# Kernel optimization log

Measured on AMD Instinct MI355X. Metric: run time of the kernel, lower is better.

## Reference

```python
import jax, jax.numpy as jnp
import numpy as np

N_ROOMS = 126          # len(building.rooms)
N = 2 + N_ROOMS        # state dim (reset_iv: 2 + n_rooms)
M = 1 + N_ROOMS        # input dim u = [Tout, Q_watts...]
T = 200000             # number of eval times
DT = 30.0              # seconds between eval points
TOUT_DT = 3600.0       # outside-temp table grid spacing (s)
K = 1700               # table length (covers 1000 + T*DT seconds)
LOAD_MAX = 500.0       # physical_loads_scaling: W/m^2 upper bound


def setup_inputs() -> dict:
    key = jax.random.key(0)
    ks = jax.random.split(key, 6)
    # Stable RC-style state matrix: negative diagonal dominates
    A = 1e-5 * jax.random.normal(ks[0], (N, N), dtype=jnp.float32) - 2e-4 * jnp.eye(N, dtype=jnp.float32)
    B = 1e-6 * jax.random.normal(ks[1], (N, M), dtype=jnp.float32)
    loads = jax.random.normal(ks[2], (2, N_ROOMS), dtype=jnp.float32)   # raw params (pre-sigmoid)
    areas = 10.0 + 40.0 * jax.random.uniform(ks[3], (N_ROOMS,), dtype=jnp.float32)  # room areas m^2
    Tout_vals = 10.0 + 5.0 * jax.random.normal(ks[4], (K,), dtype=jnp.float32)      # hourly Tout table
    t_eval = 1000.0 + DT * jnp.arange(T, dtype=jnp.float32)
    iv = 26.0 * jnp.ones((N, 1), dtype=jnp.float32)
    return {"A": A, "B": B, "loads": loads, "areas": areas,
            "Tout_vals": Tout_vals, "t_eval": t_eval, "iv": iv, "action": 1}


def _interp_tout(vals, t):
    # linear interpolation on a uniform grid starting at t=0 (replaces scipy interp1d)
    pos = t / TOUT_DT
    idx = jnp.clip(jnp.floor(pos).astype(jnp.int32), 0, K - 2)
    w = pos - idx.astype(pos.dtype)
    return vals[idx] * (1.0 - w) + vals[idx + 1] * w


def reference(A, B, loads, areas, Tout_vals, t_eval, iv, action):
    t0 = t_eval[0]
    ts = t_eval - t0
    # _build_loads: sigmoid transform + physical scaling
    lp = jax.nn.sigmoid(loads) * LOAD_MAX
    cool_load, gain_load = lp[0], lp[1]
    # f_ode constants: Q_area = -cool*action + gain; Q_watts = proportional_heating
    Q_watts = (-cool_load * action + gain_load) * areas        # [n_rooms]
    b_q = B[:, 1:] @ Q_watts                                   # [N] constant forcing
    b_T = B[:, 0]                                              # [N] Tout coupling
    x0 = iv[:, 0]

    def f(t, x):
        Tout = _interp_tout(Tout_vals, t + t0)
        return A @ x + b_T * Tout + b_q

    # torchdiffeq method='rk4' -> rk4_alt_step_func (3/8 rule)
    def step(x, tt):
        t, tn = tt
        dt = tn - t
        k1 = f(t, x)
        k2 = f(t + dt / 3.0, x + dt * k1 / 3.0)
        k3 = f(t + dt * 2.0 / 3.0, x + dt * (k2 - k1 / 3.0))
        k4 = f(t + dt, x + dt * (k1 - k2 + k3))
        xn = x + dt * (k1 + 3.0 * (k2 + k3) + k4) / 8.0
        return xn, xn

    _, traj = jax.lax.scan(step, x0, (ts[:-1], ts[1:]))
    out = jnp.concatenate([x0[None, :], traj], axis=0)         # [T, N]
    return out[..., None]                                      # [T, N, 1] matching iv shape
```

## Files before the change

### kernel.cpp

```cpp
#include <hip/hip_runtime.h>

#define N 128
#define NR 126
#define MBCOL 127
#define TSTEPS 200000
#define L1 49
#define C1 4096
#define L2 64
#define C2 64
#define KT 1700

#define OFF_Z     0
#define OFF_S     16384
#define OFF_P     32768
#define OFF_PW2   65536
#define OFF_PW4   81920
#define OFF_PW8   98304
#define OFF_PW16  114688
#define OFF_PW32  131072
#define OFF_Q     147456
#define OFF_WC    180224
#define OFF_ACC   212992
#define OFF_DELTA 737280
#define OFF_BQ    745472
#define OFF_BST   753664
#define OFF_PEH   65536
#define OFF_PEL   75776

typedef float v4f __attribute__((ext_vector_type(4)));
typedef __attribute__((ext_vector_type(8))) short bf16x8;
typedef __attribute__((ext_vector_type(4))) float f32x4;

#define GLD4(dst, p) \
  asm volatile("global_load_dwordx4 %0, %1, off" : "=v"(dst) : "v"(p))
#define PINQ(q) \
  asm volatile("s_waitcnt vmcnt(0)" \
    : "+v"(q[0]),"+v"(q[1]),"+v"(q[2]),"+v"(q[3]), \
      "+v"(q[4]),"+v"(q[5]),"+v"(q[6]),"+v"(q[7]), \
      "+v"(q[8]),"+v"(q[9]),"+v"(q[10]),"+v"(q[11]), \
      "+v"(q[12]),"+v"(q[13]),"+v"(q[14]),"+v"(q[15]))

__device__ __forceinline__ void loadQ16(v4f* qv, const float* pb)
{
  #pragma unroll
  for (int s = 0; s < 16; ++s) GLD4(qv[s], pb + 4*s);
  PINQ(qv);
}

__device__ __forceinline__ void bsplit(float f, unsigned short& h, unsigned short& l)
{
  unsigned int u = __float_as_uint(f);
  unsigned int r = (u + 0x7FFFu + ((u >> 16) & 1u)) >> 16;
  float hf = __uint_as_float(r << 16);
  h = (unsigned short)r;
  float lo = f - hf;
  unsigned int u2 = __float_as_uint(lo);
  unsigned int r2 = (u2 + 0x7FFFu + ((u2 >> 16) & 1u)) >> 16;
  l = (unsigned short)r2;
}

__global__ __launch_bounds__(128) void kPrep(
    const float* __restrict__ A, const float* __restrict__ B,
    const float* __restrict__ loads, const float* __restrict__ areas,
    const float* __restrict__ iv, const int* __restrict__ action,
    float* __restrict__ ws, float* __restrict__ out)
{
  __shared__ float qw[NR];
  __shared__ float ys[4][N];
  __shared__ float qs[4][N];
  int t = threadIdx.x;
  float actf = (float)action[0];
  if (t < NR) {
    float lc = (1.0f / (1.0f + expf(-loads[t]))) * 500.0f;
    float lg = (1.0f / (1.0f + expf(-loads[NR + t]))) * 500.0f;
    qw[t] = (-lc * actf + lg) * areas[t];
  }
  __syncthreads();
  {
    float bq = 0.0f;
    for (int i = 0; i < NR; ++i) bq += B[t * MBCOL + 1 + i] * qw[i];
    ys[0][t] = B[t * MBCOL];
    qs[0][t] = bq;
  }
  __syncthreads();
  for (int s = 1; s < 4; ++s) {
    float ay = 0.0f, aq = 0.0f;
    for (int k = 0; k < N; ++k) {
      float a = A[t * N + k];
      ay += a * ys[s-1][k];
      aq += a * qs[s-1][k];
    }
    ys[s][t] = 30.0f * ay;
    qs[s][t] = 30.0f * aq;
    __syncthreads();
  }
  float vs[5];
  vs[0] = 3.75f * (ys[0][t] + ys[1][t] + ys[2][t]*(1.0f/3.0f) + ys[3][t]*(1.0f/3.0f));
  vs[1] = 3.75f * (3.0f*ys[0][t] + 2.0f*ys[1][t] + ys[2][t]);
  vs[2] = 3.75f * (3.0f*ys[0][t] + ys[1][t]);
  vs[3] = 3.75f * ys[0][t];
  vs[4] = 3.75f * (8.0f*qs[0][t] + 4.0f*qs[1][t] + (4.0f/3.0f)*qs[2][t] + (1.0f/3.0f)*qs[3][t]);
  for (int m = 0; m < 5; ++m) ws[OFF_WC + (m*L1) * N + t] = vs[m];
  for (int i = t; i < N*N; i += 128) ws[OFF_Z + i] = 30.0f * A[i];
  out[t] = iv[t];
}

__device__ __forceinline__ void mmRow(const float* __restrict__ Aw,
                                      const float* __restrict__ Bw,
                                      float* __restrict__ Cw,
                                      float* __restrict__ Cw2,
                                      float* __restrict__ sm)
{
  int t = threadIdx.x, c = t & 127, kh = t >> 7;
  int r = blockIdx.x;
  const float* Ar = Aw + r*N + kh*64;
  const float* Bc = Bw + (kh*64)*N + c;
  float p0=0.f, p1=0.f, p2=0.f, p3=0.f;
  #pragma unroll 4
  for (int s = 0; s < 64; s += 4) {
    const float4 av = *(const float4*)(Ar + s);
    p0 = fmaf(av.x, Bc[(s+0)*N], p0);
    p1 = fmaf(av.y, Bc[(s+1)*N], p1);
    p2 = fmaf(av.z, Bc[(s+2)*N], p2);
    p3 = fmaf(av.w, Bc[(s+3)*N], p3);
  }
  sm[kh*128 + c] = (p0+p1)+(p2+p3);
  __syncthreads();
  if (kh == 0) {
    float v = sm[c] + sm[128 + c];
    Cw[r*N + c] = v;
    if (Cw2) Cw2[r*N + c] = v;
  }
}

__device__ __forceinline__ void polyRow(float* __restrict__ ws,
                                        float* __restrict__ sm)
{
  int t = threadIdx.x, c = t & 127, kh = t >> 7;
  int r = blockIdx.x;
  const float* Z = ws + OFF_Z;
  const float* S = ws + OFF_S;
  const float* Sr = S + r*N + kh*64;
  float x3=0.f, x4=0.f;
  #pragma unroll 4
  for (int s = 0; s < 64; s += 4) {
    const float4 av = *(const float4*)(Sr + s);
    int k = kh*64 + s;
    x3 = fmaf(av.x, Z[(k+0)*N+c], x3); x3 = fmaf(av.y, Z[(k+1)*N+c], x3);
    x3 = fmaf(av.z, Z[(k+2)*N+c], x3); x3 = fmaf(av.w, Z[(k+3)*N+c], x3);
    x4 = fmaf(av.x, S[(k+0)*N+c], x4); x4 = fmaf(av.y, S[(k+1)*N+c], x4);
    x4 = fmaf(av.z, S[(k+2)*N+c], x4); x4 = fmaf(av.w, S[(k+3)*N+c], x4);
  }
  sm[kh*128 + c] = x3;
  sm[256 + kh*128 + c] = x4;
  __syncthreads();
  if (kh == 0) {
    float a3 = sm[c] + sm[128+c];
    float a4 = sm[256+c] + sm[384+c];
    float pv = (r==c ? 1.0f : 0.0f) + Z[r*N+c] + 0.5f*S[r*N+c]
             + (1.0f/6.0f)*a3 + (1.0f/24.0f)*a4;
    ws[OFF_P + r*N + c] = pv;
  }
}

__device__ __forceinline__ void wUnit(const float* __restrict__ Pw,
                                      float* __restrict__ ws,
                                      int uw, int wbase, int wcount,
                                      float* __restrict__ wbuf )
{
  int t = threadIdx.x;
  int np = 5 * wcount;
  for (int i = t; i < 8*N; i += 256) {
    int pl = i >> 7, k = i & 127;
    int p = uw*8 + pl;
    float v = 0.0f;
    if (p < np) {
      int m = p / wcount, kk = p % wcount;
      v = ws[OFF_WC + (m*L1 + kk)*N + k];
    }
    wbuf[pl*N + k] = v;
  }
  __syncthreads();
  int r = t & 127, pg = t >> 7;
  float acc[4] = {0,0,0,0};
  #pragma unroll 2
  for (int k = 0; k < N; k += 4) {
    const float4 av = *(const float4*)(Pw + r*N + k);
    #pragma unroll
    for (int pi = 0; pi < 4; ++pi) {
      const float4 wv = *(const float4*)(wbuf + (pg*4+pi)*N + k);
      acc[pi] = fmaf(av.x, wv.x, acc[pi]);
      acc[pi] = fmaf(av.y, wv.y, acc[pi]);
      acc[pi] = fmaf(av.z, wv.z, acc[pi]);
      acc[pi] = fmaf(av.w, wv.w, acc[pi]);
    }
  }
  #pragma unroll
  for (int pi = 0; pi < 4; ++pi) {
    int p = uw*8 + pg*4 + pi;
    if (p < np) {
      int m = p / wcount, kk = p % wcount;
      ws[OFF_WC + (m*L1 + wbase + kk)*N + r] = acc[pi];
    }
  }
}

__global__ __launch_bounds__(256) void kPhase(float* __restrict__ ws, int ph)
{
  __shared__ float sm[1024];
  int b = blockIdx.x;
  if (ph == 1) { mmRow(ws+OFF_Z, ws+OFF_Z, ws+OFF_S, nullptr, sm); return; }
  if (ph == 2) { polyRow(ws, sm); return; }
  if (ph <= 8) {
    int s = ph - 3;
    const int srcOff[6] = {OFF_P, OFF_PW2, OFF_PW4, OFF_PW8, OFF_PW16, OFF_PW32};
    const int dstOff[6] = {OFF_PW2, OFF_PW4, OFF_PW8, OFF_PW16, OFF_PW32, OFF_S};
    if (b < 128) {
      if (s < 5) mmRow(ws+srcOff[s], ws+srcOff[s], ws+dstOff[s], nullptr, sm);
      else       mmRow(ws+OFF_PW32, ws+OFF_PW16, ws+OFF_S, nullptr, sm);
    } else {
      int wbase  = (s < 5) ? (1 << s) : 32;
      int wcount = (s < 5) ? (1 << s) : 17;
      wUnit(ws + srcOff[s], ws, b - 128, wbase, wcount, sm);
    }
    return;
  }
  if (ph == 9) {
    if (b < 128) {
      mmRow(ws+OFF_S, ws+OFF_P, ws+OFF_Z, ws+OFF_Q, sm);
    } else {
      int r = b - 128;
      int tt = threadIdx.x;
      if (tt < 160) {
        float val;
        if (tt < 128)      val = ws[OFF_P + r*N + tt];
        else if (tt < 133) val = ws[OFF_WC + ((tt-128)*L1)*N + r];
        else               val = 0.0f;
        unsigned short h, l2;
        bsplit(val, h, l2);
        ((unsigned short*)(ws + OFF_PEH))[r*160 + tt] = h;
        ((unsigned short*)(ws + OFF_PEL))[r*160 + tt] = l2;
      }
    }
    return;
  }
  {
    int d = ph - 10;
    const float* src = ws + ((d & 1) ? OFF_S : OFF_Z);
    float* dst       = ws + ((d & 1) ? OFF_Z : OFF_S);
    mmRow(src, src, dst, nullptr, sm);
  }
}

__device__ __forceinline__ void build_table(float* lt, const float* __restrict__ Tout,
                                            int J0, int t, int cnt, int stride)
{
  int tbase = 1470*J0 + 1000;
  for (int s = t; s < cnt; s += stride) {
    float tt = (float)(tbase + 10*s);
    float pos = tt / 3600.0f;
    int idx = (int)pos;
    if (idx > KT-2) idx = KT-2;
    float w = pos - (float)idx;
    lt[s] = Tout[idx]*(1.0f-w) + Tout[idx+1]*w;
  }
}

__global__ __launch_bounds__(256) void k3_acc(const float* __restrict__ Tout,
                                              float* __restrict__ ws)
{
  __shared__ float lt[1184];
  int t = threadIdx.x;
  int J0 = blockIdx.x * 8;
  build_table(lt, Tout, J0, t, 1177, 256);
  __syncthreads();
  int r = t & 127, jh = t >> 7;
  float a[4] = {0.0f, 0.0f, 0.0f, 0.0f};
  for (int k = 0; k < L1; ++k) {
    float w0 = ws[OFF_WC + (0*L1+k)*N + r];
    float w1 = ws[OFF_WC + (1*L1+k)*N + r];
    float w2 = ws[OFF_WC + (2*L1+k)*N + r];
    float w3 = ws[OFF_WC + (3*L1+k)*N + r];
    float w4 = ws[OFF_WC + (4*L1+k)*N + r];
    #pragma unroll
    for (int q = 0; q < 4; ++q) {
      int cl = jh*4 + q;
      int soff = 3*(L1*cl + (L1-1) - k);
      a[q] += w0*lt[soff] + w1*lt[soff+1] + w2*lt[soff+2] + w3*lt[soff+3] + w4;
    }
  }
  #pragma unroll
  for (int q = 0; q < 4; ++q)
    ws[OFF_ACC + (size_t)(J0 + jh*4 + q)*N + r] = a[q];
}

__device__ __forceinline__ void mv_step3(const v4f* qv, float* x, float* ps,
                                         int r, int kh, float addv)
{
  const v4f* xp = (const v4f*)(x + kh*64);
  float p0=0.f, p1=0.f, p2=0.f, p3=0.f;
  #pragma unroll
  for (int s = 0; s < 16; s += 4) {
    v4f x0 = xp[s+0], x1 = xp[s+1], x2 = xp[s+2], x3 = xp[s+3];
    p0 = fmaf(qv[s+0][0],x0[0],p0); p0 = fmaf(qv[s+0][1],x0[1],p0);
    p0 = fmaf(qv[s+0][2],x0[2],p0); p0 = fmaf(qv[s+0][3],x0[3],p0);
    p1 = fmaf(qv[s+1][0],x1[0],p1); p1 = fmaf(qv[s+1][1],x1[1],p1);
    p1 = fmaf(qv[s+1][2],x1[2],p1); p1 = fmaf(qv[s+1][3],x1[3],p1);
    p2 = fmaf(qv[s+2][0],x2[0],p2); p2 = fmaf(qv[s+2][1],x2[1],p2);
    p2 = fmaf(qv[s+2][2],x2[2],p2); p2 = fmaf(qv[s+2][3],x2[3],p2);
    p3 = fmaf(qv[s+3][0],x3[0],p3); p3 = fmaf(qv[s+3][1],x3[1],p3);
    p3 = fmaf(qv[s+3][2],x3[2],p3); p3 = fmaf(qv[s+3][3],x3[3],p3);
  }
  ps[kh*128 + r] = (p0+p1)+(p2+p3);
  __syncthreads();
  if (kh == 0) x[r] = ps[r] + ps[128 + r] + addv;
  __syncthreads();
}

__global__ __launch_bounds__(256, 2) void k4_l2a(float* __restrict__ ws)
{
  __shared__ float x[N];
  __shared__ float ps[256];
  int t = threadIdx.x, r = t & 127, kh = t >> 7;
  int q = blockIdx.x;
  v4f qv[16];
  loadQ16(qv, ws + OFF_Q + r*N + kh*64);
  if (t < N) x[t] = 0.0f;
  __syncthreads();
  float nxt = ws[OFF_ACC + (size_t)(q*L2)*N + r];
  for (int i = 0; i < L2; ++i) {
    float addv = nxt;
    if (i+1 < L2) nxt = ws[OFF_ACC + (size_t)(q*L2 + i+1)*N + r];
    mv_step3(qv, x, ps, r, kh, addv);
  }
  if (kh == 0) ws[OFF_DELTA + q*N + r] = x[r];
}

__global__ __launch_bounds__(256, 2) void k5_l3(const float* __restrict__ iv,
                                                float* __restrict__ ws)
{
  __shared__ float x[N];
  __shared__ float ps[256];
  __shared__ float dl[63*N];
  int t = threadIdx.x, r = t & 127, kh = t >> 7;
  v4f qv[16];
  loadQ16(qv, ws + OFF_Z + r*N + kh*64);
  for (int i = t; i < 63*N; i += 256) dl[i] = ws[OFF_DELTA + i];
  if (t < N) x[t] = iv[t];
  __syncthreads();
  for (int q = 0; q < C2; ++q) {
    if (kh == 0) ws[OFF_BQ + q*N + r] = x[r];
    if (q == C2-1) break;
    mv_step3(qv, x, ps, r, kh, dl[q*N + r]);
  }
}

__global__ __launch_bounds__(256, 2) void k6_l2b(float* __restrict__ ws)
{
  __shared__ float x[N];
  __shared__ float ps[256];
  int t = threadIdx.x, r = t & 127, kh = t >> 7;
  int q = blockIdx.x;
  v4f qv[16];
  loadQ16(qv, ws + OFF_Q + r*N + kh*64);
  if (t < N) x[t] = ws[OFF_BQ + q*N + t];
  __syncthreads();
  float nxt = ws[OFF_ACC + (size_t)(q*L2)*N + r];
  for (int i = 0; i < L2; ++i) {
    if (kh == 0) ws[OFF_BST + (size_t)(q*L2 + i)*N + r] = x[r];
    if (i == L2-1) break;
    float addv = nxt;
    nxt = ws[OFF_ACC + (size_t)(q*L2 + i+1)*N + r];
    mv_step3(qv, x, ps, r, kh, addv);
  }
}

__global__ __launch_bounds__(512) void k7_main(const float* __restrict__ Tout,
                                               const float* __restrict__ ws,
                                               float* __restrict__ out)
{
  __shared__ float ltp[3136];
  __shared__ __align__(16) unsigned short XbHi[16][168];
  __shared__ __align__(16) unsigned short XbLo[16][168];
  int t = threadIdx.x;
  int J0 = blockIdx.x * 16;

  for (int e = t; e < 3136; e += 512) {
    int cl = e / 196, rem = e - cl*196;
    int i = rem >> 2, m = rem & 3;
    float tt = (float)(1000 + 1470*(J0 + cl) + 30*i + 10*m);
    float pos = tt / 3600.0f;
    int idx = (int)pos;
    if (idx > KT-2) idx = KT-2;
    float w = pos - (float)idx;
    ltp[e] = Tout[idx]*(1.0f-w) + Tout[idx+1]*w;
  }
  for (int e = t; e < 2048; e += 512) {
    int cn = e >> 7, k = e & 127;
    unsigned short h, l2;
    bsplit(ws[OFF_BST + (size_t)(J0+cn)*N + k], h, l2);
    XbHi[cn][k] = h; XbLo[cn][k] = l2;
  }
  for (int e = t; e < 16*40; e += 512) {
    int cn = e / 40, k = 128 + (e - cn*40);
    XbHi[cn][k] = 0; XbLo[cn][k] = 0;
  }
  __syncthreads();
  if (t < 80) {
    int cn = t / 5, m = t - cn*5;
    float v = (m < 4) ? ltp[cn*196 + m] : 1.0f;
    unsigned short h, l2; bsplit(v, h, l2);
    XbHi[cn][128+m] = h; XbLo[cn][128+m] = l2;
  }

  int l = t & 63, w = t >> 6;
  int la = l & 15, lg = l >> 4;
  int rowA = w*16 + la;
  const unsigned short* peh = (const unsigned short*)(ws + OFF_PEH);
  const unsigned short* pel = (const unsigned short*)(ws + OFF_PEL);
  bf16x8 Ah[5], Al[5];
  #pragma unroll
  for (int kt = 0; kt < 5; ++kt) {
    Ah[kt] = *(const bf16x8*)(peh + rowA*160 + kt*32 + lg*8);
    Al[kt] = *(const bf16x8*)(pel + rowA*160 + kt*32 + lg*8);
  }
  __syncthreads();

  int rowD = w*16 + lg*4;
  int nnB = L1*(J0 + la);
  for (int i = 0; i < L1; ++i) {
    bf16x8 Bh[5], Bl[5];
    #pragma unroll
    for (int kt = 0; kt < 5; ++kt) {
      Bh[kt] = *(const bf16x8*)(&XbHi[la][kt*32 + lg*8]);
      Bl[kt] = *(const bf16x8*)(&XbLo[la][kt*32 + lg*8]);
    }
    f32x4 ahh = {0.f,0.f,0.f,0.f}, ahl = {0.f,0.f,0.f,0.f}, alh = {0.f,0.f,0.f,0.f};
    #pragma unroll
    for (int kt = 0; kt < 5; ++kt) {
      ahh = __builtin_amdgcn_mfma_f32_16x16x32_bf16(Ah[kt], Bh[kt], ahh, 0, 0, 0);
      ahl = __builtin_amdgcn_mfma_f32_16x16x32_bf16(Ah[kt], Bl[kt], ahl, 0, 0, 0);
      alh = __builtin_amdgcn_mfma_f32_16x16x32_bf16(Al[kt], Bh[kt], alh, 0, 0, 0);
    }
    f32x4 y = ahh + ahl + alh;
    int nn = nnB + i + 1;
    if (nn < TSTEPS)
      *(f32x4*)(out + (size_t)nn*N + rowD) = y;
    __syncthreads();
    unsigned short h0,h1,h2,h3,q0,q1,q2,q3;
    bsplit(y[0],h0,q0); bsplit(y[1],h1,q1); bsplit(y[2],h2,q2); bsplit(y[3],h3,q3);
    unsigned int hA = (unsigned)h0 | ((unsigned)h1<<16);
    unsigned int hB = (unsigned)h2 | ((unsigned)h3<<16);
    unsigned int lA = (unsigned)q0 | ((unsigned)q1<<16);
    unsigned int lB = (unsigned)q2 | ((unsigned)q3<<16);
    *reinterpret_cast<uint2*>(&XbHi[la][rowD]) = make_uint2(hA, hB);
    *reinterpret_cast<uint2*>(&XbLo[la][rowD]) = make_uint2(lA, lB);
    if (t < 64 && i < L1-1) {
      int cn = t >> 2, m = t & 3;
      float v = ltp[cn*196 + (i+1)*4 + m];
      unsigned short hh, ll; bsplit(v, hh, ll);
      XbHi[cn][128+m] = hh; XbLo[cn][128+m] = ll;
    }
    __syncthreads();
  }
}

extern "C" void kernel_launch(void* const* d_in, const int* in_sizes, int n_in,
                              void* d_out, int out_size, void* d_ws, size_t ws_size,
                              hipStream_t stream)
{
  const float* A     = (const float*)d_in[0];
  const float* B     = (const float*)d_in[1];
  const float* loads = (const float*)d_in[2];
  const float* areas = (const float*)d_in[3];
  const float* Tout  = (const float*)d_in[4];
  const float* iv    = (const float*)d_in[6];
  const int* action  = (const int*)d_in[7];
  float* out = (float*)d_out;
  float* ws  = (float*)d_ws;

  hipLaunchKernelGGL(kPrep, dim3(1), dim3(128), 0, stream,
                     A, B, loads, areas, iv, action, ws, out);
  const int phGrid[16] = {0, 128, 128, 129, 130, 131, 133, 138, 139,
                          256, 128, 128, 128, 128, 128, 128};
  for (int ph = 1; ph <= 15; ++ph)
    hipLaunchKernelGGL(kPhase, dim3(phGrid[ph]), dim3(256), 0, stream, ws, ph);
  hipLaunchKernelGGL(k3_acc,  dim3(512),  dim3(256), 0, stream, Tout, ws);
  hipLaunchKernelGGL(k4_l2a,  dim3(64),   dim3(256), 0, stream, ws);
  hipLaunchKernelGGL(k5_l3,   dim3(1),    dim3(256), 0, stream, iv, ws);
  hipLaunchKernelGGL(k6_l2b,  dim3(64),   dim3(256), 0, stream, ws);
  hipLaunchKernelGGL(k7_main, dim3(256),  dim3(512), 0, stream, Tout, ws, out);
}
```

Before: 262.7 us.

## Fold two squaring phases into k3/k4 blocks and use LDS-only barriers

The first two of the six squaring matmul phases now run as extra blocks inside k3_acc and k4_l2a, which removes two kernel launches and overlaps that work with the accumulation and level-2 scan. The remaining squarings run as four kPhase launches after k4, with the parity offset adjusted. __syncthreads in the serial matvec and main loops is replaced by a barrier that waits only on LDS counters (lgkmcnt), not on outstanding global loads and stores. kPrep's scaling loop is vectorised to float4. The risks are correctness: the new ordering must still deliver each power to its consumers, and the lighter barriers must not let global memory hazards through.

Result: faster. 252.0 us (-4.0%).

```diff
diff --git a/kernel.cpp b/kernel.cpp
--- a/kernel.cpp
+++ b/kernel.cpp
@@ -31,6 +31,14 @@
 typedef __attribute__((ext_vector_type(8))) short bf16x8;
 typedef __attribute__((ext_vector_type(4))) float f32x4;
 
+#define LBAR() do { \
+  __builtin_amdgcn_sched_barrier(0); \
+  asm volatile("s_waitcnt lgkmcnt(0)" ::: "memory"); \
+  __builtin_amdgcn_sched_barrier(0); \
+  __builtin_amdgcn_s_barrier(); \
+  __builtin_amdgcn_sched_barrier(0); \
+} while (0)
+
 #define GLD4(dst, p) \
   asm volatile("global_load_dwordx4 %0, %1, off" : "=v"(dst) : "v"(p))
 #define PINQ(q) \
@@ -101,18 +109,21 @@
   vs[3] = 3.75f * ys[0][t];
   vs[4] = 3.75f * (8.0f*qs[0][t] + 4.0f*qs[1][t] + (4.0f/3.0f)*qs[2][t] + (1.0f/3.0f)*qs[3][t]);
   for (int m = 0; m < 5; ++m) ws[OFF_WC + (m*L1) * N + t] = vs[m];
-  for (int i = t; i < N*N; i += 128) ws[OFF_Z + i] = 30.0f * A[i];
+  for (int i = t; i < N*N/4; i += 128) {
+    float4 a = ((const float4*)A)[i];
+    a.x *= 30.0f; a.y *= 30.0f; a.z *= 30.0f; a.w *= 30.0f;
+    ((float4*)(ws + OFF_Z))[i] = a;
+  }
   out[t] = iv[t];
 }
 
-__device__ __forceinline__ void mmRow(const float* __restrict__ Aw,
-                                      const float* __restrict__ Bw,
-                                      float* __restrict__ Cw,
-                                      float* __restrict__ Cw2,
-                                      float* __restrict__ sm)
+__device__ __forceinline__ void mmRowR(const float* __restrict__ Aw,
+                                       const float* __restrict__ Bw,
+                                       float* __restrict__ Cw,
+                                       float* __restrict__ Cw2,
+                                       float* __restrict__ sm, int r)
 {
   int t = threadIdx.x, c = t & 127, kh = t >> 7;
-  int r = blockIdx.x;
   const float* Ar = Aw + r*N + kh*64;
   const float* Bc = Bw + (kh*64)*N + c;
   float p0=0.f, p1=0.f, p2=0.f, p3=0.f;
@@ -209,15 +220,15 @@
 {
   __shared__ float sm[1024];
   int b = blockIdx.x;
-  if (ph == 1) { mmRow(ws+OFF_Z, ws+OFF_Z, ws+OFF_S, nullptr, sm); return; }
+  if (ph == 1) { mmRowR(ws+OFF_Z, ws+OFF_Z, ws+OFF_S, nullptr, sm, b); return; }
   if (ph == 2) { polyRow(ws, sm); return; }
   if (ph <= 8) {
     int s = ph - 3;
     const int srcOff[6] = {OFF_P, OFF_PW2, OFF_PW4, OFF_PW8, OFF_PW16, OFF_PW32};
     const int dstOff[6] = {OFF_PW2, OFF_PW4, OFF_PW8, OFF_PW16, OFF_PW32, OFF_S};
     if (b < 128) {
-      if (s < 5) mmRow(ws+srcOff[s], ws+srcOff[s], ws+dstOff[s], nullptr, sm);
-      else       mmRow(ws+OFF_PW32, ws+OFF_PW16, ws+OFF_S, nullptr, sm);
+      if (s < 5) mmRowR(ws+srcOff[s], ws+srcOff[s], ws+dstOff[s], nullptr, sm, b);
+      else       mmRowR(ws+OFF_PW32, ws+OFF_PW16, ws+OFF_S, nullptr, sm, b);
     } else {
       int wbase  = (s < 5) ? (1 << s) : 32;
       int wcount = (s < 5) ? (1 << s) : 17;
@@ -227,7 +238,7 @@
   }
   if (ph == 9) {
     if (b < 128) {
-      mmRow(ws+OFF_S, ws+OFF_P, ws+OFF_Z, ws+OFF_Q, sm);
+      mmRowR(ws+OFF_S, ws+OFF_P, ws+OFF_Z, ws+OFF_Q, sm, b);
     } else {
       int r = b - 128;
       int tt = threadIdx.x;
@@ -245,10 +256,10 @@
     return;
   }
   {
-    int d = ph - 10;
+    int d = ph - 8;
     const float* src = ws + ((d & 1) ? OFF_S : OFF_Z);
     float* dst       = ws + ((d & 1) ? OFF_Z : OFF_S);
-    mmRow(src, src, dst, nullptr, sm);
+    mmRowR(src, src, dst, nullptr, sm, b);
   }
 }
 
@@ -271,6 +282,10 @@
 {
   __shared__ float lt[1184];
   int t = threadIdx.x;
+  if (blockIdx.x >= 512) {
+    mmRowR(ws+OFF_Z, ws+OFF_Z, ws+OFF_S, nullptr, lt, blockIdx.x - 512);
+    return;
+  }
   int J0 = blockIdx.x * 8;
   build_table(lt, Tout, J0, t, 1177, 256);
   __syncthreads();
@@ -312,15 +327,19 @@
     p3 = fmaf(qv[s+3][2],x3[2],p3); p3 = fmaf(qv[s+3][3],x3[3],p3);
   }
   ps[kh*128 + r] = (p0+p1)+(p2+p3);
-  __syncthreads();
+  LBAR();
   if (kh == 0) x[r] = ps[r] + ps[128 + r] + addv;
-  __syncthreads();
+  LBAR();
 }
 
 __global__ __launch_bounds__(256, 2) void k4_l2a(float* __restrict__ ws)
 {
   __shared__ float x[N];
   __shared__ float ps[256];
+  if (blockIdx.x >= 64) {
+    mmRowR(ws+OFF_S, ws+OFF_S, ws+OFF_Z, nullptr, ps, blockIdx.x - 64);
+    return;
+  }
   int t = threadIdx.x, r = t & 127, kh = t >> 7;
   int q = blockIdx.x;
   v4f qv[16];
@@ -446,7 +465,7 @@
     int nn = nnB + i + 1;
     if (nn < TSTEPS)
       *(f32x4*)(out + (size_t)nn*N + rowD) = y;
-    __syncthreads();
+    LBAR();
     unsigned short h0,h1,h2,h3,q0,q1,q2,q3;
     bsplit(y[0],h0,q0); bsplit(y[1],h1,q1); bsplit(y[2],h2,q2); bsplit(y[3],h3,q3);
     unsigned int hA = (unsigned)h0 | ((unsigned)h1<<16);
@@ -461,7 +480,7 @@
       unsigned short hh, ll; bsplit(v, hh, ll);
       XbHi[cn][128+m] = hh; XbLo[cn][128+m] = ll;
     }
-    __syncthreads();
+    LBAR();
   }
 }
 
@@ -481,12 +500,13 @@
 
   hipLaunchKernelGGL(kPrep, dim3(1), dim3(128), 0, stream,
                      A, B, loads, areas, iv, action, ws, out);
-  const int phGrid[16] = {0, 128, 128, 129, 130, 131, 133, 138, 139,
-                          256, 128, 128, 128, 128, 128, 128};
-  for (int ph = 1; ph <= 15; ++ph)
+  const int phGrid[10] = {0, 128, 128, 129, 130, 131, 133, 138, 139, 256};
+  for (int ph = 1; ph <= 9; ++ph)
     hipLaunchKernelGGL(kPhase, dim3(phGrid[ph]), dim3(256), 0, stream, ws, ph);
-  hipLaunchKernelGGL(k3_acc,  dim3(512),  dim3(256), 0, stream, Tout, ws);
-  hipLaunchKernelGGL(k4_l2a,  dim3(64),   dim3(256), 0, stream, ws);
+  hipLaunchKernelGGL(k3_acc,  dim3(640),  dim3(256), 0, stream, Tout, ws);
+  hipLaunchKernelGGL(k4_l2a,  dim3(192),  dim3(256), 0, stream, ws);
+  for (int ph = 10; ph <= 13; ++ph)
+    hipLaunchKernelGGL(kPhase, dim3(128), dim3(256), 0, stream, ws, ph);
   hipLaunchKernelGGL(k5_l3,   dim3(1),    dim3(256), 0, stream, iv, ws);
   hipLaunchKernelGGL(k6_l2b,  dim3(64),   dim3(256), 0, stream, ws);
   hipLaunchKernelGGL(k7_main, dim3(256),  dim3(512), 0, stream, Tout, ws, out);
```
